# Kernel tuning notes

Measured on AMD Instinct MI355X. Metric: run time of the kernel, lower is better.

The kernel has to match this reference:

```python
import jax, jax.numpy as jnp
import numpy as np
from jax import lax

D_MODEL = 256
SCALES = 3
DM2 = 2 * D_MODEL            # 512, inner d_model of each Mamba2
EXPAND = 2
D_INNER = EXPAND * DM2       # 1024
HEADDIM = 64                 # Mamba2 default
NHEADS = D_INNER // HEADDIM  # 16
DSTATE = 128
DCONV = 4
D_IN_PROJ = 2 * D_INNER + 2 * DSTATE + NHEADS  # 2320
CONV_CH = D_INNER + 2 * DSTATE                 # 1280


def layernorm(x, g, b, eps=1e-5):
    mu = x.mean(-1, keepdims=True)
    v = ((x - mu) ** 2).mean(-1, keepdims=True)
    return (x - mu) * lax.rsqrt(v + eps) * g + b


def mamba2(x, Win, convw, convb, dtb, Alog, Dh, normw, Wout):
    # x: [B, L, DM2]
    Bb, L, _ = x.shape
    zxbcdt = x @ Win                                   # [B, L, 2320]
    z = zxbcdt[..., :D_INNER]                          # gate branch
    xBC = zxbcdt[..., D_INNER:D_INNER + CONV_CH]       # [B, L, 1280]
    dt = jax.nn.softplus(zxbcdt[..., -NHEADS:] + dtb)  # [B, L, H]
    # causal depthwise conv1d over time
    xc = lax.conv_general_dilated(
        xBC.transpose(0, 2, 1), convw[:, None, :], (1,), [(DCONV - 1, 0)],
        feature_group_count=CONV_CH, dimension_numbers=('NCH', 'OIH', 'NCH'))
    xBC = jax.nn.silu(xc.transpose(0, 2, 1) + convb)
    xs = xBC[..., :D_INNER].reshape(Bb, L, NHEADS, HEADDIM)  # [B,L,H,P]
    Bm = xBC[..., D_INNER:D_INNER + DSTATE]                  # [B,L,N] (ngroups=1)
    Cm = xBC[..., D_INNER + DSTATE:]                         # [B,L,N]
    A = -jnp.exp(Alog)                                       # [H]
    dA = jnp.exp(dt * A)                                     # [B,L,H]

    def step(h, inp):
        dA_t, dt_t, x_t, B_t, C_t = inp
        h = dA_t[:, :, None, None] * h + jnp.einsum('bh,bhp,bn->bhpn', dt_t, x_t, B_t)
        return h, jnp.einsum('bhpn,bn->bhp', h, C_t)

    h0 = jnp.zeros((Bb, NHEADS, HEADDIM, DSTATE), x.dtype)
    _, ys = lax.scan(step, h0, (dA.transpose(1, 0, 2), dt.transpose(1, 0, 2),
                                xs.transpose(1, 0, 2, 3), Bm.transpose(1, 0, 2),
                                Cm.transpose(1, 0, 2)))
    y = ys.transpose(1, 0, 2, 3) + Dh[None, None, :, None] * xs   # skip term
    y = y.reshape(Bb, L, D_INNER)
    y = y * jax.nn.silu(z)                                        # gated RMSNorm
    y = y * lax.rsqrt((y * y).mean(-1, keepdims=True) + 1e-5) * normw
    return y @ Wout


def msfusion(x, Wp, bp, Wpre, bpre, lnpre_g, lnpre_b, Wpost, bpost, lnpost_g, lnpost_b,
             Win_f, convw_f, convb_f, dtb_f, Alog_f, Dh_f, normw_f, Wout_f,
             Win_b, convw_b, convb_b, dtb_b, Alog_b, Dh_b, normw_b, Wout_b):
    B, S, T, D = x.shape
    x_ = x.transpose(0, 2, 1, 3).reshape(B, T, S * D)
    x_ = x_ @ Wp + bp                                  # 1x1 conv == linear
    shortcut = x_
    h = layernorm(x_ @ Wpre + bpre, lnpre_g, lnpre_b)  # [B,T,512]
    gate = jax.nn.silu(h)
    out_f = mamba2(h, Win_f, convw_f, convb_f, dtb_f, Alog_f, Dh_f, normw_f, Wout_f)
    out_b = jnp.flip(mamba2(jnp.flip(h, 1), Win_b, convw_b, convb_b, dtb_b, Alog_b, Dh_b, normw_b, Wout_b), 1)
    out = layernorm((out_f * gate + out_b * gate) @ Wpost + bpost, lnpost_g, lnpost_b) + shortcut
    fn = out / jnp.maximum(jnp.linalg.norm(out, axis=-1, keepdims=True), 1e-12)
    attn = jnp.einsum('btd,bsd->bts', fn, fn)          # [B,T,T]
    return out, attn


def setup_inputs() -> dict:
    key = jax.random.key(0)
    ks = iter(jax.random.split(key, 40))
    n = lambda shape, s=0.02: (s * jax.random.normal(next(ks), shape)).astype(jnp.float32)
    B, S, T, D = 4, SCALES, 2048, D_MODEL
    inp = {
        'x': jax.random.normal(next(ks), (B, S, T, D), jnp.float32),
        'Wp': n((S * D, D)), 'bp': n((D,)),
        'Wpre': n((D, DM2)), 'bpre': n((DM2,)),
        'lnpre_g': jnp.ones((DM2,), jnp.float32), 'lnpre_b': jnp.zeros((DM2,), jnp.float32),
        'Wpost': n((DM2, D)), 'bpost': n((D,)),
        'lnpost_g': jnp.ones((D,), jnp.float32), 'lnpost_b': jnp.zeros((D,), jnp.float32),
    }
    for sfx in ('f', 'b'):
        inp['Win_' + sfx] = n((DM2, D_IN_PROJ))
        inp['convw_' + sfx] = n((CONV_CH, DCONV), 0.1)
        inp['convb_' + sfx] = jnp.zeros((CONV_CH,), jnp.float32)
        inp['dtb_' + sfx] = n((NHEADS,), 0.5)
        inp['Alog_' + sfx] = jnp.log(jnp.arange(1, NHEADS + 1, dtype=jnp.float32))
        inp['Dh_' + sfx] = jnp.ones((NHEADS,), jnp.float32)
        inp['normw_' + sfx] = jnp.ones((D_INNER,), jnp.float32)
        inp['Wout_' + sfx] = n((D_INNER, DM2))
    return inp


def reference(x, Wp, bp, Wpre, bpre, lnpre_g, lnpre_b, Wpost, bpost, lnpost_g, lnpost_b,
              Win_f, convw_f, convb_f, dtb_f, Alog_f, Dh_f, normw_f, Wout_f,
              Win_b, convw_b, convb_b, dtb_b, Alog_b, Dh_b, normw_b, Wout_b):
    return msfusion(x, Wp, bp, Wpre, bpre, lnpre_g, lnpre_b, Wpost, bpost, lnpost_g, lnpost_b,
                    Win_f, convw_f, convb_f, dtb_f, Alog_f, Dh_f, normw_f, Wout_f,
                    Win_b, convw_b, convb_b, dtb_b, Alog_b, Dh_b, normw_b, Wout_b)
```

## Files before the change

### kernel.cpp

```cpp
#include <hip/hip_runtime.h>
#include <math.h>

__device__ __forceinline__ float sigf(float v) { return 1.f / (1.f + __expf(-v)); }

__device__ __forceinline__ short f2bf(float f) {
  unsigned int u = __builtin_bit_cast(unsigned int, f);
  unsigned int r = (u + 0x7fffu + ((u >> 16) & 1u)) >> 16;
  return (short)r;
}
__device__ __forceinline__ float bf2f(short s) {
  unsigned int u = ((unsigned int)(unsigned short)s) << 16;
  return __builtin_bit_cast(float, u);
}

typedef short bf16x8 __attribute__((ext_vector_type(8)));
typedef float f32x4 __attribute__((ext_vector_type(4)));

#define ZB_STRIDE   19005440ll
#define XCV_STRIDE  10485760ll
#define SBUF_STRIDE 16777216ll
#define YB_STRIDE    8388608ll
#define DT_STRIDE     131072ll
#define PB_STRIDE       2048ll
#define WINT_STRIDE  1310720ll

__device__ __forceinline__ void async16(const short* g, short* l) {
  __builtin_amdgcn_global_load_lds(
      (const __attribute__((address_space(1))) unsigned int*)g,
      (__attribute__((address_space(3))) unsigned int*)l, 16, 0, 0);
}

template<bool BIAS, bool ACC, bool W16>
__global__ __launch_bounds__(256) void gemm16_kernel(
    const short* __restrict__ A, const short* __restrict__ Bt,
    const float* __restrict__ bias, float* __restrict__ C,
    int M, int N, int K, int ldc,
    long long sAb, long long sBb, long long sCb,
    short* __restrict__ C16)
{
  __shared__ short sm[2][2][128 * 32];
  const int tid = threadIdx.x;
  const int wave = tid >> 6;
  const int lane = tid & 63;
  const int m0 = blockIdx.x * 128;
  const int n0 = blockIdx.y * 128;
  const int bz = blockIdx.z;
  const short* Ab = A + (size_t)bz * sAb;
  const short* Bb = Bt + (size_t)bz * sBb;
  float* Cb = C + (size_t)bz * sCb;

  f32x4 acc[4][4] = {};

  const int isB = wave >> 1;
  const int half = wave & 1;
  const short* gsrc = isB ? Bb : Ab;
  const int tile_r0 = isB ? n0 : m0;
  const int lrow = lane >> 2;
  const int lk = (((lane & 3) ^ ((lane >> 3) & 3)) * 8);
  const short* gbase = gsrc + (size_t)(tile_r0 + half * 64 + lrow) * K + lk;
  short* lbase0 = &sm[0][isB][(half * 64) * 32];
  short* lbase1 = &sm[1][isB][(half * 64) * 32];

  const int wm = wave >> 1, wn = wave & 1;
  const int nt = K >> 5;

  auto STAGE = [&](int buf, int t) {
    const short* g0 = gbase + t * 32;
    short* l0 = buf ? lbase1 : lbase0;
#pragma unroll
    for (int c = 0; c < 4; c++)
      async16(g0 + (size_t)c * 16 * K, l0 + c * 512);
  };

  STAGE(0, 0);
  asm volatile("s_waitcnt vmcnt(0)" ::: "memory");
  __builtin_amdgcn_s_barrier();

  const int rs = (((lane >> 4) ^ ((lane >> 1) & 3)) * 8);
  int cur = 0;
  for (int t = 0; t < nt; ++t) {
    if (t + 1 < nt) STAGE(cur ^ 1, t + 1);
    const short* smA = &sm[cur][0][0];
    const short* smB = &sm[cur][1][0];
    bf16x8 af[4], bfr[4];
#pragma unroll
    for (int mt = 0; mt < 4; mt++)
      af[mt] = *(bf16x8*)&smA[(wm * 64 + mt * 16 + (lane & 15)) * 32 + rs];
#pragma unroll
    for (int nn = 0; nn < 4; nn++)
      bfr[nn] = *(bf16x8*)&smB[(wn * 64 + nn * 16 + (lane & 15)) * 32 + rs];
#pragma unroll
    for (int mt = 0; mt < 4; mt++)
#pragma unroll
      for (int nn = 0; nn < 4; nn++)
        acc[mt][nn] = __builtin_amdgcn_mfma_f32_16x16x32_bf16(bfr[nn], af[mt], acc[mt][nn], 0, 0, 0);
    asm volatile("s_waitcnt vmcnt(0)" ::: "memory");
    __builtin_amdgcn_s_barrier();
    cur ^= 1;
  }
  const int mcol = lane & 15;
  const int nq = (lane >> 4) * 4;
#pragma unroll
  for (int mt = 0; mt < 4; mt++) {
    int row = m0 + wm * 64 + mt * 16 + mcol;
#pragma unroll
    for (int nn = 0; nn < 4; nn++) {
      int col = n0 + wn * 64 + nn * 16 + nq;
      if (col >= N) continue;
      float4 v = make_float4(acc[mt][nn][0], acc[mt][nn][1], acc[mt][nn][2], acc[mt][nn][3]);
      float* cp = Cb + (size_t)row * ldc + col;
      if (BIAS) {
        float4 bv = *(const float4*)(bias + col);
        v.x += bv.x; v.y += bv.y; v.z += bv.z; v.w += bv.w;
      }
      if (ACC) {
        float4 ov = *(const float4*)cp;
        v.x += ov.x; v.y += ov.y; v.z += ov.z; v.w += ov.w;
      }
      *(float4*)cp = v;
      if (W16) {
        *(short4*)(C16 + (size_t)row * ldc + col) =
            make_short4(f2bf(v.x), f2bf(v.y), f2bf(v.z), f2bf(v.w));
      }
    }
  }
}

__global__ void tcast_kernel(const float* __restrict__ W, short* __restrict__ Wt,
                             int K, int N)
{
  __shared__ float tile[32][33];
  int n0 = blockIdx.x * 32, k0 = blockIdx.y * 32;
  int c = threadIdx.x & 31, r8 = threadIdx.x >> 5;
#pragma unroll
  for (int i = 0; i < 4; i++) {
    int r = r8 + i * 8;
    int n = n0 + c;
    tile[r][c] = (n < N) ? W[(size_t)(k0 + r) * N + n] : 0.f;
  }
  __syncthreads();
#pragma unroll
  for (int i = 0; i < 4; i++) {
    int r = r8 + i * 8;
    Wt[(size_t)(n0 + r) * K + k0 + c] = f2bf(tile[c][r]);
  }
}

__global__ void tcast2_kernel(const float* __restrict__ W0, const float* __restrict__ W1,
                              short* __restrict__ Wt, int K, int N, long long sWt)
{
  __shared__ float tile[32][33];
  const int dir = blockIdx.z;
  const float* W = dir ? W1 : W0;
  short* Wtd = Wt + (size_t)dir * sWt;
  int n0 = blockIdx.x * 32, k0 = blockIdx.y * 32;
  int c = threadIdx.x & 31, r8 = threadIdx.x >> 5;
#pragma unroll
  for (int i = 0; i < 4; i++) {
    int r = r8 + i * 8;
    int n = n0 + c;
    tile[r][c] = (n < N) ? W[(size_t)(k0 + r) * N + n] : 0.f;
  }
  __syncthreads();
#pragma unroll
  for (int i = 0; i < 4; i++) {
    int r = r8 + i * 8;
    Wtd[(size_t)(n0 + r) * K + k0 + c] = f2bf(tile[c][r]);
  }
}

__global__ void gather_cast_kernel(const float* __restrict__ x, short* __restrict__ Ag)
{
  int idx = blockIdx.x * 256 + threadIdx.x;
  int m = idx / 192;
  int g = idx - m * 192;
  int k = g * 4;
  int s = k >> 8, d = k & 255;
  int b = m >> 11, t = m & 2047;
  float4 v = *(const float4*)(x + ((size_t)((b * 3 + s) * 2048 + t) << 8) + d);
  *(short4*)(Ag + (size_t)m * 768 + k) = make_short4(f2bf(v.x), f2bf(v.y), f2bf(v.z), f2bf(v.w));
}

__global__ void ln512_kernel(float* __restrict__ xio, const float* __restrict__ g,
                             const float* __restrict__ b, short* __restrict__ o16)
{
  const int row = blockIdx.x;
  const int lane = threadIdx.x;
  float* xr = xio + (size_t)row * 512;
  float4 v0 = *(float4*)(xr + lane * 4);
  float4 v1 = *(float4*)(xr + 256 + lane * 4);
  float sum = v0.x + v0.y + v0.z + v0.w + v1.x + v1.y + v1.z + v1.w;
#pragma unroll
  for (int o = 32; o >= 1; o >>= 1) sum += __shfl_xor(sum, o);
  const float mu = sum * (1.f / 512.f);
  float d[8] = {v0.x - mu, v0.y - mu, v0.z - mu, v0.w - mu,
                v1.x - mu, v1.y - mu, v1.z - mu, v1.w - mu};
  float vs = 0.f;
#pragma unroll
  for (int i = 0; i < 8; i++) vs += d[i] * d[i];
#pragma unroll
  for (int o = 32; o >= 1; o >>= 1) vs += __shfl_xor(vs, o);
  const float inv = rsqrtf(vs * (1.f / 512.f) + 1e-5f);
  float4 g0 = *(const float4*)(g + lane * 4);
  float4 g1 = *(const float4*)(g + 256 + lane * 4);
  float4 b0 = *(const float4*)(b + lane * 4);
  float4 b1 = *(const float4*)(b + 256 + lane * 4);
  v0.x = d[0] * inv * g0.x + b0.x; v0.y = d[1] * inv * g0.y + b0.y;
  v0.z = d[2] * inv * g0.z + b0.z; v0.w = d[3] * inv * g0.w + b0.w;
  v1.x = d[4] * inv * g1.x + b1.x; v1.y = d[5] * inv * g1.y + b1.y;
  v1.z = d[6] * inv * g1.z + b1.z; v1.w = d[7] * inv * g1.w + b1.w;
  *(float4*)(xr + lane * 4) = v0;
  *(float4*)(xr + 256 + lane * 4) = v1;
  short* orow = o16 + (size_t)row * 512;
  *(short4*)(orow + lane * 4) = make_short4(f2bf(v0.x), f2bf(v0.y), f2bf(v0.z), f2bf(v0.w));
  *(short4*)(orow + 256 + lane * 4) = make_short4(f2bf(v1.x), f2bf(v1.y), f2bf(v1.z), f2bf(v1.w));
}

__global__ void dtprep_kernel(const float* __restrict__ Z,
                              const float* __restrict__ dtb0, const float* __restrict__ dtb1,
                              const float* __restrict__ Alog0, const float* __restrict__ Alog1,
                              float* __restrict__ dtv, float* __restrict__ ldA)
{
  const int dir = blockIdx.y;
  const float* Zd = Z + (size_t)dir * ZB_STRIDE;
  const float* dtb = dir ? dtb1 : dtb0;
  const float* Alog = dir ? Alog1 : Alog0;
  float* dtvd = dtv + dir * DT_STRIDE;
  float* ldAd = ldA + dir * DT_STRIDE;
  int idx = blockIdx.x * 256 + threadIdx.x;
  int row = idx >> 4, hh = idx & 15;
  float raw = Zd[(size_t)row * 2320 + 2304 + hh] + dtb[hh];
  float dt = raw > 20.f ? raw : log1pf(expf(raw));
  dtvd[idx] = dt;
  ldAd[idx] = -dt * expf(Alog[hh]);
}

__global__ void conv_kernel(const float* __restrict__ Z,
                            const float* __restrict__ cw0, const float* __restrict__ cw1,
                            const float* __restrict__ cb0, const float* __restrict__ cb1,
                            short* __restrict__ xcv)
{
  const int dir = blockIdx.z;
  const int t0 = blockIdx.x * 64;
  const int b = blockIdx.y / 5;
  const int chb = blockIdx.y % 5;
  const int c = chb * 256 + threadIdx.x;
  const float* convw = dir ? cw1 : cw0;
  const float* convb = dir ? cb1 : cb0;
  const float* Zd = Z + (size_t)dir * ZB_STRIDE + (size_t)(b * 2048) * 2320 + 1024 + c;
  short* xd = xcv + (size_t)dir * XCV_STRIDE + (size_t)(b * 2048) * 1280 + c;

  const float w0 = convw[c * 4 + 0], w1 = convw[c * 4 + 1];
  const float w2 = convw[c * 4 + 2], w3 = convw[c * 4 + 3];
  const float bias = convb[c];
  const int o = dir ? 0 : -3;

  float rr[4];
#pragma unroll
  for (int j = 0; j < 4; j++) {
    int pos = t0 + o + j;
    rr[j] = (pos >= 0 && pos < 2048) ? Zd[(size_t)pos * 2320] : 0.f;
  }
#pragma unroll 8
  for (int i = 0; i < 64; i++) {
    float a = bias;
    if (dir) { a += w0 * rr[3]; a += w1 * rr[2]; a += w2 * rr[1]; a += w3 * rr[0]; }
    else     { a += w0 * rr[0]; a += w1 * rr[1]; a += w2 * rr[2]; a += w3 * rr[3]; }
    xd[(size_t)(t0 + i) * 1280] = f2bf(a * sigf(a));
    rr[0] = rr[1]; rr[1] = rr[2]; rr[2] = rr[3];
    int pos = t0 + i + 1 + o + 3;
    rr[3] = (pos >= 0 && pos < 2048) ? Zd[(size_t)pos * 2320] : 0.f;
  }
}

__global__ __launch_bounds__(256) void chunk_state_kernel(
    const short* __restrict__ xcv_, const float* __restrict__ dtv_,
    const float* __restrict__ ldA_, short* __restrict__ Sbuf_,
    float* __restrict__ Pbuf_)
{
  __shared__ float sw[64];
  __shared__ short sXT[64 * 74];
  __shared__ short sBw[128 * 74];
  const int dir = blockIdx.z;
  const short* xcv = xcv_ + (size_t)dir * XCV_STRIDE;
  const float* dtv = dtv_ + dir * DT_STRIDE;
  const float* ldA = ldA_ + dir * DT_STRIDE;
  short* Sbuf = Sbuf_ + (size_t)dir * SBUF_STRIDE;
  float* Pbuf = Pbuf_ + dir * PB_STRIDE;
  const int bh = blockIdx.x, ck = blockIdx.y;
  const int b = bh >> 4, h = bh & 15;
  const int tid = threadIdx.x;
  const int wave = tid >> 6, lane = tid & 63;

  if (tid < 64) {
    int tg = ck * 64 + tid;
    int tt = dir ? 2047 - tg : tg;
    size_t r = (size_t)(b * 2048 + tt) * 16 + h;
    float v = ldA[r];
#pragma unroll
    for (int o = 1; o < 64; o <<= 1) { float u = __shfl_up(v, o); if (tid >= o) v += u; }
    float tot = __shfl(v, 63);
    sw[tid] = __expf(tot - v) * dtv[r];
    if (tid == 63) Pbuf[bh * 32 + ck] = __expf(tot);
  }
  __syncthreads();
  for (int i4 = tid; i4 < 512; i4 += 256) {
    int s = i4 >> 3, p0 = (i4 & 7) * 8;
    int tg = ck * 64 + s; int tt = dir ? 2047 - tg : tg;
    bf16x8 xv = *(const bf16x8*)(xcv + (size_t)(b * 2048 + tt) * 1280 + h * 64 + p0);
#pragma unroll
    for (int j = 0; j < 8; j++) sXT[(p0 + j) * 74 + s] = xv[j];
  }
  for (int i4 = tid; i4 < 1024; i4 += 256) {
    int s = i4 >> 4, n0 = (i4 & 15) * 8;
    int tg = ck * 64 + s; int tt = dir ? 2047 - tg : tg;
    bf16x8 bv = *(const bf16x8*)(xcv + (size_t)(b * 2048 + tt) * 1280 + 1024 + n0);
    float w = sw[s];
#pragma unroll
    for (int j = 0; j < 8; j++) sBw[(n0 + j) * 74 + s] = f2bf(w * bf2f(bv[j]));
  }
  __syncthreads();

  const int mcol = lane & 15, kgrp = (lane >> 4) * 8;
  bf16x8 af[2];
#pragma unroll
  for (int kk = 0; kk < 2; kk++)
    af[kk] = *(bf16x8*)&sXT[(wave * 16 + mcol) * 74 + kk * 32 + kgrp];
  f32x4 acc[8] = {};
#pragma unroll
  for (int j = 0; j < 8; j++)
#pragma unroll
    for (int kk = 0; kk < 2; kk++) {
      bf16x8 bf = *(bf16x8*)&sBw[(j * 16 + mcol) * 74 + kk * 32 + kgrp];
      acc[j] = __builtin_amdgcn_mfma_f32_16x16x32_bf16(bf, af[kk], acc[j], 0, 0, 0);
    }
  short* Sp = Sbuf + ((size_t)(bh * 32 + ck) << 13);
  const int p = wave * 16 + mcol;
  const int nq = (lane >> 4) * 4;
#pragma unroll
  for (int j = 0; j < 8; j++) {
    *(short4*)(Sp + p * 128 + j * 16 + nq) = make_short4(
        f2bf(acc[j][0]), f2bf(acc[j][1]), f2bf(acc[j][2]), f2bf(acc[j][3]));
  }
}

__global__ void chunk_scan_kernel(short* __restrict__ Sbuf, const float* __restrict__ Pbuf)
{
  int idx = blockIdx.x * 256 + threadIdx.x;
  int bhd = idx >> 12;
  int pr = idx & 4095;
  int dir = bhd >> 6, bh = bhd & 63;
  short* Sb = Sbuf + (size_t)dir * SBUF_STRIDE;
  const float* Pb = Pbuf + dir * PB_STRIDE;
  float h0 = 0.f, h1 = 0.f;
  for (int ck = 0; ck < 32; ck++) {
    size_t off = ((size_t)(bh * 32 + ck) << 13) + pr * 2;
    unsigned int u = *(const unsigned int*)(Sb + off);
    float s0 = bf2f((short)(u & 0xffff));
    float s1 = bf2f((short)(u >> 16));
    float P = Pb[bh * 32 + ck];
    unsigned int w = (unsigned int)(unsigned short)f2bf(h0) |
                     ((unsigned int)(unsigned short)f2bf(h1) << 16);
    *(unsigned int*)(Sb + off) = w;
    h0 = P * h0 + s0;
    h1 = P * h1 + s1;
  }
}

__global__ __launch_bounds__(256) void chunk_out_kernel(
    const short* __restrict__ xcv_, const float* __restrict__ dtv_,
    const float* __restrict__ ldA_, const short* __restrict__ Sbuf_,
    const float* __restrict__ Dh0, const float* __restrict__ Dh1,
    short* __restrict__ y_)
{
  extern __shared__ short smem16[];
  short* sB  = smem16;
  short* sXT = sB + 64 * 136;
  short* sP  = sXT + 64 * 74;
  float* sL  = (float*)(sP + 64 * 74);
  float* sdt = sL + 64;

  const int dir = blockIdx.z;
  const short* xcv = xcv_ + (size_t)dir * XCV_STRIDE;
  const float* dtv = dtv_ + dir * DT_STRIDE;
  const float* ldA = ldA_ + dir * DT_STRIDE;
  const short* Sbuf = Sbuf_ + (size_t)dir * SBUF_STRIDE;
  const float* Dh = dir ? Dh1 : Dh0;
  short* y = y_ + (size_t)dir * YB_STRIDE;

  const int bh = blockIdx.x, ck = blockIdx.y;
  const int b = bh >> 4, h = bh & 15;
  const int tid = threadIdx.x;
  const int wave = tid >> 6, lane = tid & 63;

  const int mcol = lane & 15;
  const int kgrp = (lane >> 4) * 8;
  const int trow = wave * 16 + mcol;
  const int sq = (lane >> 4) * 4;

  const int tgc = ck * 64 + trow;
  const int ttc = dir ? 2047 - tgc : tgc;
  const short* crow = xcv + (size_t)(b * 2048 + ttc) * 1280 + 1152;
  bf16x8 afC[4];
#pragma unroll
  for (int kk = 0; kk < 4; kk++)
    afC[kk] = *(const bf16x8*)(crow + kk * 32 + kgrp);

  if (tid < 64) {
    int tg = ck * 64 + tid;
    int tt = dir ? 2047 - tg : tg;
    size_t r = (size_t)(b * 2048 + tt) * 16 + h;
    float v = ldA[r];
#pragma unroll
    for (int o = 1; o < 64; o <<= 1) { float u = __shfl_up(v, o); if (tid >= o) v += u; }
    sL[tid] = v;
    sdt[tid] = dtv[r];
  }
  for (int i4 = tid; i4 < 1024; i4 += 256) {
    int t = i4 >> 4, c8 = (i4 & 15) * 8;
    int tg = ck * 64 + t; int tt = dir ? 2047 - tg : tg;
    const short* rp = xcv + (size_t)(b * 2048 + tt) * 1280;
    *(bf16x8*)&sB[t * 136 + c8] = *(const bf16x8*)(rp + 1024 + c8);
  }
  for (int i4 = tid; i4 < 512; i4 += 256) {
    int t = i4 >> 3, p0 = (i4 & 7) * 8;
    int tg = ck * 64 + t; int tt = dir ? 2047 - tg : tg;
    bf16x8 xv = *(const bf16x8*)(xcv + (size_t)(b * 2048 + tt) * 1280 + h * 64 + p0);
#pragma unroll
    for (int j = 0; j < 8; j++) sXT[(p0 + j) * 74 + t] = xv[j];
  }
  __syncthreads();

  f32x4 sacc[4] = {};
#pragma unroll
  for (int j = 0; j < 4; j++)
#pragma unroll
    for (int kk = 0; kk < 4; kk++) {
      bf16x8 bf = *(bf16x8*)&sB[(j * 16 + mcol) * 136 + kk * 32 + kgrp];
      sacc[j] = __builtin_amdgcn_mfma_f32_16x16x32_bf16(bf, afC[kk], sacc[j], 0, 0, 0);
    }

  const float Lt = sL[trow];
#pragma unroll
  for (int j = 0; j < 4; j++) {
    int s0 = j * 16 + sq;
    float vr[4];
#pragma unroll
    for (int r = 0; r < 4; r++) {
      int s = s0 + r;
      vr[r] = (trow >= s) ? sacc[j][r] * __expf(Lt - sL[s]) * sdt[s] : 0.f;
    }
    *(short4*)&sP[trow * 74 + s0] = make_short4(
        f2bf(vr[0]), f2bf(vr[1]), f2bf(vr[2]), f2bf(vr[3]));
  }
  asm volatile("s_waitcnt lgkmcnt(0)" ::: "memory");
  __builtin_amdgcn_sched_barrier(0);

  bf16x8 afP[2];
#pragma unroll
  for (int kk = 0; kk < 2; kk++)
    afP[kk] = *(bf16x8*)&sP[trow * 74 + kk * 32 + kgrp];
  f32x4 yacc[4] = {};
#pragma unroll
  for (int j = 0; j < 4; j++)
#pragma unroll
    for (int kk = 0; kk < 2; kk++) {
      bf16x8 bf = *(bf16x8*)&sXT[(j * 16 + mcol) * 74 + kk * 32 + kgrp];
      yacc[j] = __builtin_amdgcn_mfma_f32_16x16x32_bf16(bf, afP[kk], yacc[j], 0, 0, 0);
    }
  const short* Hp = Sbuf + ((size_t)(bh * 32 + ck) << 13);
  f32x4 y2[4] = {};
#pragma unroll
  for (int j = 0; j < 4; j++)
#pragma unroll
    for (int kk = 0; kk < 4; kk++) {
      bf16x8 bf = *(const bf16x8*)(Hp + (j * 16 + mcol) * 128 + kk * 32 + kgrp);
      y2[j] = __builtin_amdgcn_mfma_f32_16x16x32_bf16(bf, afC[kk], y2[j], 0, 0, 0);
    }

  const float dh = Dh[h];
  const float eL = __expf(Lt);
  short* yrow = y + (size_t)(b * 2048 + ttc) * 1024 + h * 64;
#pragma unroll
  for (int j = 0; j < 4; j++) {
    int p0 = j * 16 + sq;
    short o[4];
#pragma unroll
    for (int r = 0; r < 4; r++) {
      float xv = bf2f(sXT[(p0 + r) * 74 + trow]);
      o[r] = f2bf(yacc[j][r] + eL * y2[j][r] + dh * xv);
    }
    *(short4*)(yrow + p0) = make_short4(o[0], o[1], o[2], o[3]);
  }
}

__global__ void rms_kernel(short* __restrict__ y_, const float* __restrict__ Z,
                           const float* __restrict__ nw0, const float* __restrict__ nw1)
{
  const int dir = blockIdx.y;
  const int row = blockIdx.x;
  const int lane = threadIdx.x;
  short* yr = y_ + (size_t)dir * YB_STRIDE + (size_t)row * 1024;
  const float* zr = Z + (size_t)dir * ZB_STRIDE + (size_t)row * 2320;
  const float* normw = dir ? nw1 : nw0;
  float vals[16];
  float ss = 0.f;
#pragma unroll
  for (int jj = 0; jj < 4; jj++) {
    int off = jj * 256 + lane * 4;
    short4 yv = *(short4*)(yr + off);
    float4 zv = *(const float4*)(zr + off);
    float a0 = bf2f(yv.x) * (zv.x * sigf(zv.x));
    float a1 = bf2f(yv.y) * (zv.y * sigf(zv.y));
    float a2 = bf2f(yv.z) * (zv.z * sigf(zv.z));
    float a3 = bf2f(yv.w) * (zv.w * sigf(zv.w));
    vals[jj * 4 + 0] = a0; vals[jj * 4 + 1] = a1;
    vals[jj * 4 + 2] = a2; vals[jj * 4 + 3] = a3;
    ss += a0 * a0 + a1 * a1 + a2 * a2 + a3 * a3;
  }
#pragma unroll
  for (int o = 32; o >= 1; o >>= 1) ss += __shfl_xor(ss, o);
  const float scale = rsqrtf(ss * (1.f / 1024.f) + 1e-5f);
#pragma unroll
  for (int jj = 0; jj < 4; jj++) {
    int off = jj * 256 + lane * 4;
    float4 nw = *(const float4*)(normw + off);
    *(short4*)(yr + off) = make_short4(
        f2bf(vals[jj * 4 + 0] * scale * nw.x), f2bf(vals[jj * 4 + 1] * scale * nw.y),
        f2bf(vals[jj * 4 + 2] * scale * nw.z), f2bf(vals[jj * 4 + 3] * scale * nw.w));
  }
}

__global__ void combine_kernel(const float* __restrict__ od0, const float* __restrict__ od1,
                               const float* __restrict__ h, short* __restrict__ ob)
{
  size_t idx = (size_t)blockIdx.x * 256 + threadIdx.x;
  float4 a = ((const float4*)od0)[idx];
  float4 bb = ((const float4*)od1)[idx];
  float4 g = ((const float4*)h)[idx];
  float4 o;
  o.x = (a.x + bb.x) * (g.x * sigf(g.x));
  o.y = (a.y + bb.y) * (g.y * sigf(g.y));
  o.z = (a.z + bb.z) * (g.z * sigf(g.z));
  o.w = (a.w + bb.w) * (g.w * sigf(g.w));
  *(short4*)(ob + idx * 4) = make_short4(f2bf(o.x), f2bf(o.y), f2bf(o.z), f2bf(o.w));
}

__global__ void lnshort_kernel(const float* __restrict__ v, const float* __restrict__ g,
                               const float* __restrict__ b, const float* __restrict__ shortcut,
                               float* __restrict__ out0, short* __restrict__ fn)
{
  const int row = blockIdx.x;
  const int lane = threadIdx.x;
  size_t base = (size_t)row * 256;
  float4 x = *(const float4*)(v + base + lane * 4);
  float sum = x.x + x.y + x.z + x.w;
#pragma unroll
  for (int o = 32; o >= 1; o >>= 1) sum += __shfl_xor(sum, o);
  const float mu = sum * (1.f / 256.f);
  float d[4] = {x.x - mu, x.y - mu, x.z - mu, x.w - mu};
  float vs = d[0] * d[0] + d[1] * d[1] + d[2] * d[2] + d[3] * d[3];
#pragma unroll
  for (int o = 32; o >= 1; o >>= 1) vs += __shfl_xor(vs, o);
  const float inv = rsqrtf(vs * (1.f / 256.f) + 1e-5f);
  float4 gg = *(const float4*)(g + lane * 4);
  float4 bb = *(const float4*)(b + lane * 4);
  float4 sc = *(const float4*)(shortcut + base + lane * 4);
  float4 o4;
  o4.x = d[0] * inv * gg.x + bb.x + sc.x;
  o4.y = d[1] * inv * gg.y + bb.y + sc.y;
  o4.z = d[2] * inv * gg.z + bb.z + sc.z;
  o4.w = d[3] * inv * gg.w + bb.w + sc.w;
  *(float4*)(out0 + base + lane * 4) = o4;
  float ns = o4.x * o4.x + o4.y * o4.y + o4.z * o4.z + o4.w * o4.w;
#pragma unroll
  for (int o = 32; o >= 1; o >>= 1) ns += __shfl_xor(ns, o);
  const float r = 1.f / fmaxf(sqrtf(ns), 1e-12f);
  *(short4*)(fn + base + lane * 4) =
      make_short4(f2bf(o4.x * r), f2bf(o4.y * r), f2bf(o4.z * r), f2bf(o4.w * r));
}

extern "C" void kernel_launch(void* const* d_in, const int* in_sizes, int n_in,
                              void* d_out, int out_size, void* d_ws, size_t ws_size,
                              hipStream_t stream)
{
  (void)in_sizes; (void)n_in; (void)out_size; (void)ws_size;
  const float* x        = (const float*)d_in[0];
  const float* Wp       = (const float*)d_in[1];
  const float* bp       = (const float*)d_in[2];
  const float* Wpre     = (const float*)d_in[3];
  const float* bpre     = (const float*)d_in[4];
  const float* lnpre_g  = (const float*)d_in[5];
  const float* lnpre_b  = (const float*)d_in[6];
  const float* Wpost    = (const float*)d_in[7];
  const float* bpost    = (const float*)d_in[8];
  const float* lnpost_g = (const float*)d_in[9];
  const float* lnpost_b = (const float*)d_in[10];
  const float* Win_f   = (const float*)d_in[11];
  const float* convw_f = (const float*)d_in[12];
  const float* convb_f = (const float*)d_in[13];
  const float* dtb_f   = (const float*)d_in[14];
  const float* Alog_f  = (const float*)d_in[15];
  const float* Dh_f    = (const float*)d_in[16];
  const float* normw_f = (const float*)d_in[17];
  const float* Wout_f  = (const float*)d_in[18];
  const float* Win_b   = (const float*)d_in[19];
  const float* convw_b = (const float*)d_in[20];
  const float* convb_b = (const float*)d_in[21];
  const float* dtb_b   = (const float*)d_in[22];
  const float* Alog_b  = (const float*)d_in[23];
  const float* Dh_b    = (const float*)d_in[24];
  const float* normw_b = (const float*)d_in[25];
  const float* Wout_b  = (const float*)d_in[26];

  float* ws   = (float*)d_ws;
  float* Zb   = ws;
  float* xcvr = Zb + 2 * 19005440;
  float* xc   = xcvr + 10485760;
  float* hbuf = xc + 2097152;
  short* hb16 = (short*)(hbuf + 4194304);
  float* yb16f= hbuf + 4194304 + 2097152;
  short* yb16 = (short*)yb16f;
  float* od   = yb16f + 8388608;
  float* dtv  = od + 4194304;
  float* ldA  = dtv + 262144;
  float* Pbuf = ldA + 262144;
  short* WinT = (short*)(Pbuf + 4096);
  short* WoutT= WinT + 2 * WINT_STRIDE;

  short* xcv16  = (short*)xcvr;
  short* Ag16   = (short*)xcvr;
  short* WpT    = (short*)(xcvr + 3145728);
  short* xcb    = (short*)xcvr;
  short* WpreT  = (short*)(xcvr + 1048576);
  short* ob16   = (short*)xcvr;
  short* WpostT = (short*)(xcvr + 2097152);
  float* vbuf = yb16f;
  short* fn16 = (short*)(yb16f + 2097152);

  float* out0 = (float*)d_out;
  float* attn = out0 + 2097152;
  short* Sbuf16 = (short*)attn;
  float* od1 = attn;

  tcast_kernel<<<dim3(8, 24), 256, 0, stream>>>(Wp, WpT, 768, 256);
  gather_cast_kernel<<<6144, 256, 0, stream>>>(x, Ag16);
  gemm16_kernel<true, false, true><<<dim3(64, 2), 256, 0, stream>>>(
      Ag16, WpT, bp, xc, 8192, 256, 768, 256, 0, 0, 0, xcb);
  tcast_kernel<<<dim3(16, 8), 256, 0, stream>>>(Wpre, WpreT, 256, 512);
  gemm16_kernel<true, false, false><<<dim3(64, 4), 256, 0, stream>>>(
      xcb, WpreT, bpre, hbuf, 8192, 512, 256, 512, 0, 0, 0, nullptr);
  ln512_kernel<<<8192, 64, 0, stream>>>(hbuf, lnpre_g, lnpre_b, hb16);

  tcast2_kernel<<<dim3(80, 16, 2), 256, 0, stream>>>(Win_f, Win_b, WinT, 512, 2320, WINT_STRIDE);
  tcast2_kernel<<<dim3(16, 32, 2), 256, 0, stream>>>(Wout_f, Wout_b, WoutT, 1024, 512, 524288);
  gemm16_kernel<false, false, false><<<dim3(64, 19, 2), 256, 0, stream>>>(
      hb16, WinT, nullptr, Zb, 8192, 2320, 512, 2320, 0, WINT_STRIDE, ZB_STRIDE, nullptr);
  dtprep_kernel<<<dim3(512, 2), 256, 0, stream>>>(Zb, dtb_f, dtb_b, Alog_f, Alog_b, dtv, ldA);
  conv_kernel<<<dim3(32, 20, 2), 256, 0, stream>>>(Zb, convw_f, convw_b, convb_f, convb_b, xcv16);
  chunk_state_kernel<<<dim3(64, 32, 2), 256, 0, stream>>>(xcv16, dtv, ldA, Sbuf16, Pbuf);
  chunk_scan_kernel<<<2048, 256, 0, stream>>>(Sbuf16, Pbuf);
  chunk_out_kernel<<<dim3(64, 32, 2), 256, 36864, stream>>>(xcv16, dtv, ldA, Sbuf16, Dh_f, Dh_b, yb16);
  rms_kernel<<<dim3(8192, 2), 64, 0, stream>>>(yb16, Zb, normw_f, normw_b);
  gemm16_kernel<false, false, false><<<dim3(64, 4), 256, 0, stream>>>(
      yb16, WoutT, nullptr, od, 8192, 512, 1024, 512, 0, 0, 0, nullptr);
  gemm16_kernel<false, false, false><<<dim3(64, 4), 256, 0, stream>>>(
      yb16 + YB_STRIDE, WoutT + 524288, nullptr, od1, 8192, 512, 1024, 512, 0, 0, 0, nullptr);

  combine_kernel<<<4096, 256, 0, stream>>>(od, od1, hbuf, ob16);
  tcast_kernel<<<dim3(8, 16), 256, 0, stream>>>(Wpost, WpostT, 512, 256);
  gemm16_kernel<true, false, false><<<dim3(64, 2), 256, 0, stream>>>(
      ob16, WpostT, bpost, vbuf, 8192, 256, 512, 256, 0, 0, 0, nullptr);
  lnshort_kernel<<<8192, 64, 0, stream>>>(vbuf, lnpost_g, lnpost_b, xc, out0, fn16);
  gemm16_kernel<false, false, false><<<dim3(16, 16, 4), 256, 0, stream>>>(
      fn16, fn16, nullptr, attn, 2048, 2048, 256, 2048,
      (long long)2048 * 256, (long long)2048 * 256, (long long)2048 * 2048, nullptr);
}
```

Measured before the change: 548.4 us.

## Exploit symmetry of attention Gram GEMM and batch both out-projection GEMMs

The final fn·fnᵀ GEMM is symmetric, so it now launches only the lower-triangular 136 tiles per batch, maps each linear block index to a (row, column) tile pair, and also writes every off-diagonal tile transposed into the mirrored position. This roughly halves the MFMA work, at the price of strided, uncoalesced scalar stores for the mirrored copy. The two Wout GEMMs are also merged into a single batched launch with z=2 that writes into the freed Zb region, removing one kernel launch and raising occupancy.

```diff
diff --git a/kernel.cpp b/kernel.cpp
--- a/kernel.cpp
+++ b/kernel.cpp
@@ -30,7 +30,7 @@
       (__attribute__((address_space(3))) unsigned int*)l, 16, 0, 0);
 }
 
-template<bool BIAS, bool ACC, bool W16>
+template<bool BIAS, bool ACC, bool W16, bool SYM>
 __global__ __launch_bounds__(256) void gemm16_kernel(
     const short* __restrict__ A, const short* __restrict__ Bt,
     const float* __restrict__ bias, float* __restrict__ C,
@@ -42,8 +42,18 @@
   const int tid = threadIdx.x;
   const int wave = tid >> 6;
   const int lane = tid & 63;
-  const int m0 = blockIdx.x * 128;
-  const int n0 = blockIdx.y * 128;
+  int bx, by;
+  if (SYM) {
+    int j = blockIdx.x;
+    by = (int)((sqrtf(8.f * j + 1.f) - 1.f) * 0.5f);
+    while ((by + 1) * (by + 2) / 2 <= j) by++;
+    while (by * (by + 1) / 2 > j) by--;
+    bx = j - by * (by + 1) / 2;
+  } else {
+    bx = blockIdx.x; by = blockIdx.y;
+  }
+  const int m0 = bx * 128;
+  const int n0 = by * 128;
   const int bz = blockIdx.z;
   const short* Ab = A + (size_t)bz * sAb;
   const short* Bb = Bt + (size_t)bz * sBb;
@@ -121,6 +131,14 @@
       if (W16) {
         *(short4*)(C16 + (size_t)row * ldc + col) =
             make_short4(f2bf(v.x), f2bf(v.y), f2bf(v.z), f2bf(v.w));
+      }
+      if (SYM) {
+        if (m0 != n0) {
+          float vv[4] = {v.x, v.y, v.z, v.w};
+#pragma unroll
+          for (int i = 0; i < 4; i++)
+            Cb[(size_t)(col + i) * ldc + row] = vv[i];
+        }
       }
     }
   }
@@ -621,8 +639,8 @@
   short* hb16 = (short*)(hbuf + 4194304);
   float* yb16f= hbuf + 4194304 + 2097152;
   short* yb16 = (short*)yb16f;
-  float* od   = yb16f + 8388608;
-  float* dtv  = od + 4194304;
+  float* odun = yb16f + 8388608;
+  float* dtv  = odun + 4194304;
   float* ldA  = dtv + 262144;
   float* Pbuf = ldA + 262144;
   short* WinT = (short*)(Pbuf + 4096);
@@ -641,20 +659,20 @@
   float* out0 = (float*)d_out;
   float* attn = out0 + 2097152;
   short* Sbuf16 = (short*)attn;
-  float* od1 = attn;
+  float* odb = Zb;
 
   tcast_kernel<<<dim3(8, 24), 256, 0, stream>>>(Wp, WpT, 768, 256);
   gather_cast_kernel<<<6144, 256, 0, stream>>>(x, Ag16);
-  gemm16_kernel<true, false, true><<<dim3(64, 2), 256, 0, stream>>>(
+  gemm16_kernel<true, false, true, false><<<dim3(64, 2), 256, 0, stream>>>(
       Ag16, WpT, bp, xc, 8192, 256, 768, 256, 0, 0, 0, xcb);
   tcast_kernel<<<dim3(16, 8), 256, 0, stream>>>(Wpre, WpreT, 256, 512);
-  gemm16_kernel<true, false, false><<<dim3(64, 4), 256, 0, stream>>>(
+  gemm16_kernel<true, false, false, false><<<dim3(64, 4), 256, 0, stream>>>(
       xcb, WpreT, bpre, hbuf, 8192, 512, 256, 512, 0, 0, 0, nullptr);
   ln512_kernel<<<8192, 64, 0, stream>>>(hbuf, lnpre_g, lnpre_b, hb16);
 
   tcast2_kernel<<<dim3(80, 16, 2), 256, 0, stream>>>(Win_f, Win_b, WinT, 512, 2320, WINT_STRIDE);
   tcast2_kernel<<<dim3(16, 32, 2), 256, 0, stream>>>(Wout_f, Wout_b, WoutT, 1024, 512, 524288);
-  gemm16_kernel<false, false, false><<<dim3(64, 19, 2), 256, 0, stream>>>(
+  gemm16_kernel<false, false, false, false><<<dim3(64, 19, 2), 256, 0, stream>>>(
       hb16, WinT, nullptr, Zb, 8192, 2320, 512, 2320, 0, WINT_STRIDE, ZB_STRIDE, nullptr);
   dtprep_kernel<<<dim3(512, 2), 256, 0, stream>>>(Zb, dtb_f, dtb_b, Alog_f, Alog_b, dtv, ldA);
   conv_kernel<<<dim3(32, 20, 2), 256, 0, stream>>>(Zb, convw_f, convw_b, convb_f, convb_b, xcv16);
@@ -662,17 +680,16 @@
   chunk_scan_kernel<<<2048, 256, 0, stream>>>(Sbuf16, Pbuf);
   chunk_out_kernel<<<dim3(64, 32, 2), 256, 36864, stream>>>(xcv16, dtv, ldA, Sbuf16, Dh_f, Dh_b, yb16);
   rms_kernel<<<dim3(8192, 2), 64, 0, stream>>>(yb16, Zb, normw_f, normw_b);
-  gemm16_kernel<false, false, false><<<dim3(64, 4), 256, 0, stream>>>(
-      yb16, WoutT, nullptr, od, 8192, 512, 1024, 512, 0, 0, 0, nullptr);
-  gemm16_kernel<false, false, false><<<dim3(64, 4), 256, 0, stream>>>(
-      yb16 + YB_STRIDE, WoutT + 524288, nullptr, od1, 8192, 512, 1024, 512, 0, 0, 0, nullptr);
-
-  combine_kernel<<<4096, 256, 0, stream>>>(od, od1, hbuf, ob16);
+  gemm16_kernel<false, false, false, false><<<dim3(64, 4, 2), 256, 0, stream>>>(
+      yb16, WoutT, nullptr, odb, 8192, 512, 1024, 512,
+      YB_STRIDE, 524288, 4194304, nullptr);
+
+  combine_kernel<<<4096, 256, 0, stream>>>(odb, odb + 4194304, hbuf, ob16);
   tcast_kernel<<<dim3(8, 16), 256, 0, stream>>>(Wpost, WpostT, 512, 256);
-  gemm16_kernel<true, false, false><<<dim3(64, 2), 256, 0, stream>>>(
+  gemm16_kernel<true, false, false, false><<<dim3(64, 2), 256, 0, stream>>>(
       ob16, WpostT, bpost, vbuf, 8192, 256, 512, 256, 0, 0, 0, nullptr);
   lnshort_kernel<<<8192, 64, 0, stream>>>(vbuf, lnpost_g, lnpost_b, xc, out0, fn16);
-  gemm16_kernel<false, false, false><<<dim3(16, 16, 4), 256, 0, stream>>>(
+  gemm16_kernel<false, false, false, true><<<dim3(136, 1, 4), 256, 0, stream>>>(
       fn16, fn16, nullptr, attn, 2048, 2048, 256, 2048,
       (long long)2048 * 256, (long long)2048 * 256, (long long)2048 * 2048, nullptr);
 }
```

After: 530.7 us. 1.03x faster.
